# Kernel optimization log

Hardware: AMD Instinct MI355X
Metric: run time of the kernel (lower is better)

## Reference

```python
import jax, jax.numpy as jnp
import numpy as np
from jax import lax

N_ENT, N_REL, N_TYPE = 50000, 237, 4000
DE, NOUT, DT = 100, 128, 200
N_EDGE, B = 800000, 4096
ALPHA, EPS = 0.2, 1e-5
NUM_FILT, FILT_W = 32, 9
FC_LEN = ((NOUT - FILT_W) // 2 + 1 - 2) // 2 + 1  # width after conv(s=2) then pool(2,s=2)
FC_LEN = FC_LEN * NUM_FILT  # height stays 1 -> 30*32 = 960


def setup_inputs() -> dict:
    key = jax.random.key(0)
    ks = jax.random.split(key, 16)
    inp = {
        'x_batch': jax.random.randint(ks[0], (B,), 0, N_ENT),
        'edge_index': jax.random.randint(ks[1], (2, N_EDGE), 0, N_ENT),
        'edge_type': jax.random.randint(ks[2], (N_EDGE,), 0, N_REL),
        'E_w': jax.random.normal(ks[3], (N_ENT, DE)) * 0.05,
        'R_w': jax.random.normal(ks[4], (N_REL, DE)) * 0.05,
        'T_w': jax.random.normal(ks[5], (N_TYPE, DT)) * 0.05,
        'W_f': jax.random.normal(ks[6], (DE, NOUT)) * (1.0 / np.sqrt(DE)),
        'a_vec': jax.random.normal(ks[7], (2 * NOUT,)) * 0.05,
        'conv_w': jax.random.normal(ks[8], (NUM_FILT, 1, 1, FILT_W)) * 0.1,
        'conv_b': jnp.zeros((NUM_FILT,)),
        'bn1_g': jnp.ones((1,)), 'bn1_b': jnp.zeros((1,)),
        'bn3_g': jnp.ones((NUM_FILT,)), 'bn3_b': jnp.zeros((NUM_FILT,)),
        'bn2_g': jnp.ones((DT,)), 'bn2_b': jnp.zeros((DT,)),
        'fc_w': jax.random.normal(ks[9], (DT, FC_LEN)) * (1.0 / np.sqrt(FC_LEN)),
        'fc_b': jnp.zeros((DT,)),
        'b_bias': jnp.zeros((N_TYPE,)),
    }
    return inp


def _bn(x, g, b, axes):
    # training-mode batch norm (biased variance), broadcastable g/b
    mean = jnp.mean(x, axis=axes, keepdims=True)
    var = jnp.var(x, axis=axes, keepdims=True)
    return g * (x - mean) * lax.rsqrt(var + EPS) + b


def _frgat(E_w, R_w, edge_index, edge_type, W_f, a_vec):
    src, dst = edge_index[0], edge_index[1]
    h = E_w @ W_f                                   # [N, NOUT]
    comp = E_w[src] - R_w[edge_type]                # 'sub' composition, [E, DE]
    m = comp @ W_f                                  # messages, [E, NOUT]
    score = jnp.concatenate([h[dst], m], axis=1) @ a_vec  # [E]
    score = jax.nn.leaky_relu(score, ALPHA)
    smax = jax.ops.segment_max(score, dst, num_segments=N_ENT)
    ex = jnp.exp(score - smax[dst])
    denom = jax.ops.segment_sum(ex, dst, num_segments=N_ENT)
    att = ex / (denom[dst] + 1e-16)
    agg = jax.ops.segment_sum(att[:, None] * m, dst, num_segments=N_ENT)
    return jax.nn.elu(agg)                          # F.elu on out_att output


def reference(x_batch, edge_index, edge_type, E_w, R_w, T_w, W_f, a_vec,
              conv_w, conv_b, bn1_g, bn1_b, bn3_g, bn3_b, bn2_g, bn2_b,
              fc_w, fc_b, b_bias):
    ent = _frgat(E_w, R_w, edge_index, edge_type, W_f, a_vec)   # [N, NOUT]
    e = ent[x_batch].reshape(B, 1, 1, NOUT)                     # NCHW
    x = _bn(e, bn1_g.reshape(1, 1, 1, 1), bn1_b.reshape(1, 1, 1, 1), (0, 2, 3))
    x = lax.conv_general_dilated(x, conv_w, window_strides=(2, 2), padding='VALID',
                                 dimension_numbers=('NCHW', 'OIHW', 'NCHW'))
    x = x + conv_b.reshape(1, -1, 1, 1)
    x = _bn(x, bn3_g.reshape(1, -1, 1, 1), bn3_b.reshape(1, -1, 1, 1), (0, 2, 3))
    x = jax.nn.relu(x)
    x = lax.reduce_window(x, -jnp.inf, lax.max, (1, 1, 1, 2), (1, 1, 2, 2), 'VALID')
    x = x.reshape(B, -1)                                        # [B, FC_LEN]
    x = x @ fc_w.T + fc_b
    x = _bn(x, bn2_g[None, :], bn2_b[None, :], (0,))
    x = jax.nn.relu(x)
    logits = x @ T_w.T + b_bias
    return jax.nn.sigmoid(logits)
```

## Files before the change

### kernel.cpp

```cpp
#include <hip/hip_runtime.h>
#include <hip/hip_bf16.h>
#include <math.h>

#define N_ENT   50000
#define N_REL   237
#define N_TYPE  4000
#define DE      100
#define NOUT    128
#define DT      200
#define N_EDGE  800000
#define B_SZ    4096
#define ALPHA   0.2f
#define EPS     1e-5f
#define NUM_FILT 32
#define CONV_W_OUT 60
#define POOL_W  30
#define FC_LEN  960
#define KP      224

typedef unsigned short ushort_t;
typedef __attribute__((ext_vector_type(8))) short bf16x8;
typedef __attribute__((ext_vector_type(4))) float f32x4;

__global__ void k_fill0(float4* p, int n) {
    int i = blockIdx.x * blockDim.x + threadIdx.x;
    if (i < n) p[i] = make_float4(0.f, 0.f, 0.f, 0.f);
}

__global__ void k_fillconst(float* p, long n, float val) {
    long i = (long)blockIdx.x * blockDim.x + threadIdx.x;
    long stride = (long)gridDim.x * blockDim.x;
    for (; i < n; i += stride) p[i] = val;
}

__global__ void k_flags(const int* xb, int* flags) {
    int i = blockIdx.x * blockDim.x + threadIdx.x;
    if (i < B_SZ) flags[xb[i]] = 1;
}

__global__ void k_slots(int* flags, int* counter, int* slotent) {
    int i = blockIdx.x * blockDim.x + threadIdx.x;
    if (i >= N_ENT) return;
    if (flags[i]) {
        int s = atomicAdd(counter, 1);
        flags[i] = 1 + s;
        slotent[s] = i;
    }
}

__global__ void k_prep(const float* Wf, const float* a_vec, const float* Rw,
                       float* wa1, float* wa2, float* rw) {
    __shared__ float sa[2 * NOUT];
    __shared__ float swa2[DE];
    int t = threadIdx.x;
    sa[t] = a_vec[t];
    __syncthreads();
    if (t < DE) {
        float s1 = 0.f, s2 = 0.f;
        for (int j = 0; j < NOUT; j++) {
            float w = Wf[t * NOUT + j];
            s1 += w * sa[j];
            s2 += w * sa[NOUT + j];
        }
        wa1[t] = s1; wa2[t] = s2; swa2[t] = s2;
    }
    __syncthreads();
    if (t < N_REL) {
        float s = 0.f;
        for (int k = 0; k < DE; k++) s += Rw[t * DE + k] * swa2[k];
        rw[t] = s;
    }
}

__global__ void k_entdots(const float* Ew, const float* wa1, const float* wa2,
                          float* ha, float* ew) {
    int wid = blockIdx.x * 4 + (threadIdx.x >> 6);
    int lane = threadIdx.x & 63;
    if (wid >= N_ENT) return;
    float s1 = 0.f, s2 = 0.f;
    if (lane < DE / 2) {
        const float2* p = (const float2*)(Ew + (size_t)wid * DE);
        float2 v = p[lane];
        s1 = v.x * wa1[2 * lane] + v.y * wa1[2 * lane + 1];
        s2 = v.x * wa2[2 * lane] + v.y * wa2[2 * lane + 1];
    }
    for (int off = 32; off > 0; off >>= 1) {
        s1 += __shfl_down(s1, off);
        s2 += __shfl_down(s2, off);
    }
    if (lane == 0) { ha[wid] = s1; ew[wid] = s2; }
}

__global__ void k_count(const int* ei, const int* flags, int* ecount) {
    int e = blockIdx.x * blockDim.x + threadIdx.x;
    if (e >= N_EDGE) return;
    int s = flags[ei[N_EDGE + e]];
    if (s) atomicAdd(&ecount[s - 1], 1);
}

__global__ void k_scan(const int* ecount, int* eoff, int* epos) {
    __shared__ int loc[4096];
    __shared__ int tot[256];
    int t = threadIdx.x;
    int base = t * 16;
    int run = 0;
    for (int i = 0; i < 16; i++) { loc[base + i] = run; run += ecount[base + i]; }
    tot[t] = run;
    __syncthreads();
    for (int off = 1; off < 256; off <<= 1) {
        int u = (t >= off) ? tot[t - off] : 0;
        __syncthreads();
        tot[t] += u;
        __syncthreads();
    }
    int ex = tot[t] - run;
    for (int i = 0; i < 16; i++) {
        int o = ex + loc[base + i];
        eoff[base + i] = o;
        epos[base + i] = o;
    }
}

__global__ void k_scatter(const int* ei, const int* et, const int* flags,
                          int* epos, int2* ebuck) {
    int e = blockIdx.x * blockDim.x + threadIdx.x;
    if (e >= N_EDGE) return;
    int s = flags[ei[N_EDGE + e]];
    if (!s) return;
    int idx = atomicAdd(&epos[s - 1], 1);
    ebuck[idx] = make_int2(ei[e], et[e]);
}

__global__ void k_agg(const int* counter, const int* ecount, const int* eoff,
                      const int* slotent, const int2* ebuck,
                      const float* Ew, const float* Rw,
                      const float* ha, const float* ew, const float* rw,
                      float* aggc) {
    int slot = blockIdx.x;
    if (slot >= counter[0]) return;
    int t = threadIdx.x;
    int n = ecount[slot], o = eoff[slot];
    float hae = ha[slotent[slot]];
    float acc = 0.f, den = 0.f;
    for (int j = 0; j < n; j++) {
        int2 p = ebuck[o + j];
        float sc = hae + ew[p.x] - rw[p.y];
        sc = sc >= 0.f ? sc : ALPHA * sc;
        float ex = expf(sc);
        den += ex;
        if (t < DE) acc += ex * (Ew[(size_t)p.x * DE + t] - Rw[(size_t)p.y * DE + t]);
    }
    if (t < DE) aggc[(size_t)slot * DE + t] = acc / (den + 1e-16f);
}

__global__ void k_gatherconv(const int* xb, const int* flags, const float* aggc,
                             const float* Wf, const float* convw,
                             float* ebuf, float* gps, float* gpq, float* cpart) {
    __shared__ float row[DE];
    __shared__ float xs[NOUT];
    __shared__ float cw[NUM_FILT * 9];
    __shared__ float red[NOUT], red2[NOUT];
    int b = blockIdx.x, t = threadIdx.x;
    int slot = flags[xb[b]] - 1;
    if (t < DE) row[t] = aggc[(size_t)slot * DE + t];
    for (int i = t; i < NUM_FILT * 9; i += 128) cw[i] = convw[i];
    __syncthreads();
    float acc = 0.f;
    for (int k = 0; k < DE; k++) acc += row[k] * Wf[k * NOUT + t];
    float x = acc > 0.f ? acc : expm1f(acc);
    xs[t] = x;
    ebuf[(size_t)b * NOUT + t] = x;
    red[t] = x; red2[t] = x * x;
    __syncthreads();
    for (int s = 64; s > 0; s >>= 1) {
        if (t < s) { red[t] += red[t + s]; red2[t] += red2[t + s]; }
        __syncthreads();
    }
    if (t == 0) { gps[b] = red[0]; gpq[b] = red2[0]; }
    int c = t >> 2, wg = t & 3;
    float ls = 0.f, lq = 0.f;
    for (int i = 0; i < 15; i++) {
        int w = wg + 4 * i;
        float u = 0.f;
        #pragma unroll
        for (int j = 0; j < 9; j++) u += cw[c * 9 + j] * xs[2 * w + j];
        ls += u; lq += u * u;
    }
    __syncthreads();
    red[t] = ls; red2[t] = lq;
    __syncthreads();
    if (wg == 0) {
        float s = red[t] + red[t + 1] + red[t + 2] + red[t + 3];
        float q = red2[t] + red2[t + 1] + red2[t + 2] + red2[t + 3];
        cpart[b * 64 + c] = s;
        cpart[b * 64 + 32 + c] = q;
    }
}

__global__ void k_red1(const float* gps, const float* gpq, const float* g1, float* bn1stat) {
    __shared__ float r1[256], r2[256];
    int t = threadIdx.x;
    float s = 0.f, q = 0.f;
    for (int b = t; b < B_SZ; b += 256) { s += gps[b]; q += gpq[b]; }
    r1[t] = s; r2[t] = q;
    __syncthreads();
    for (int k = 128; k > 0; k >>= 1) {
        if (t < k) { r1[t] += r1[t + k]; r2[t] += r2[t + k]; }
        __syncthreads();
    }
    if (t == 0) {
        float N = (float)(B_SZ * NOUT);
        float mean = r1[0] / N;
        float var = r2[0] / N - mean * mean;
        bn1stat[2] = g1[0] * rsqrtf(var + EPS);
    }
}

__global__ void k_redAB(const float* cpart, const float* bn1stat,
                        const float* g3, const float* b3, float* AB) {
    __shared__ float r1[256], r2[256];
    int c = blockIdx.x, t = threadIdx.x;
    float s = 0.f, q = 0.f;
    for (int b = t; b < B_SZ; b += 256) { s += cpart[b * 64 + c]; q += cpart[b * 64 + 32 + c]; }
    r1[t] = s; r2[t] = q;
    __syncthreads();
    for (int k = 128; k > 0; k >>= 1) {
        if (t < k) { r1[t] += r1[t + k]; r2[t] += r2[t + k]; }
        __syncthreads();
    }
    if (t == 0) {
        float N = (float)(B_SZ * CONV_W_OUT);
        float mu = r1[0] / N;
        float vu = r2[0] / N - mu * mu;
        float s1 = bn1stat[2];
        float A = g3[c] * s1 * rsqrtf(s1 * s1 * vu + EPS);
        AB[c] = A;
        AB[32 + c] = b3[c] - A * mu;
    }
}

__global__ void k_pool(const float* ebuf, const float* convw, const float* AB,
                       __hip_bfloat16* pooled) {
    __shared__ float xs[NOUT];
    __shared__ float cw[NUM_FILT * 9];
    __shared__ float sA[32], sB[32];
    int b = blockIdx.x, t = threadIdx.x;
    xs[t] = ebuf[(size_t)b * NOUT + t];
    for (int i = t; i < NUM_FILT * 9; i += 128) cw[i] = convw[i];
    if (t < 32) { sA[t] = AB[t]; sB[t] = AB[32 + t]; }
    __syncthreads();
    int c = t >> 2, wg = t & 3;
    float A = sA[c], Bv = sB[c];
    for (int i = 0; i < 8; i++) {
        int w2 = wg + 4 * i;
        if (w2 < POOL_W) {
            int w = 2 * w2;
            float u0 = 0.f, u1 = 0.f;
            #pragma unroll
            for (int j = 0; j < 9; j++) {
                float cv = cw[c * 9 + j];
                u0 += cv * xs[2 * w + j];
                u1 += cv * xs[2 * w + 2 + j];
            }
            float z0 = fmaxf(A * u0 + Bv, 0.f);
            float z1 = fmaxf(A * u1 + Bv, 0.f);
            pooled[((size_t)b * NUM_FILT + c) * POOL_W + w2] = __float2bfloat16(fmaxf(z0, z1));
        }
    }
}

__global__ void k_pad_fcw(const float* fcw, __hip_bfloat16* bfc) {
    int i = blockIdx.x * blockDim.x + threadIdx.x;
    if (i >= KP * FC_LEN) return;
    bfc[i] = __float2bfloat16((i < DT * FC_LEN) ? fcw[i] : 0.f);
}

__global__ void k_pad_tw(const float* tw, __hip_bfloat16* b2) {
    int i = blockIdx.x * blockDim.x + threadIdx.x;
    if (i >= N_TYPE * KP) return;
    int n = i / KP, k = i - n * KP;
    b2[i] = __float2bfloat16((k < DT) ? tw[n * DT + k] : 0.f);
}

template<int MODE>
__launch_bounds__(256)
__global__ void k_gemm(const ushort_t* A, const ushort_t* Bm, const float* bias,
                       int K, int ldc, int nbias, float* Cf) {
    int wave = threadIdx.x >> 6, lane = threadIdx.x & 63;
    int m0 = blockIdx.x * 128 + wave * 32;
    int n0 = blockIdx.y * 32;
    int rsel = lane & 15, ksel = (lane >> 4) * 8;
    const ushort_t* pa0 = A + (size_t)(m0 + rsel) * K + ksel;
    const ushort_t* pa1 = pa0 + (size_t)16 * K;
    const ushort_t* pb0 = Bm + (size_t)(n0 + rsel) * K + ksel;
    const ushort_t* pb1 = pb0 + (size_t)16 * K;
    f32x4 acc00 = {0.f, 0.f, 0.f, 0.f};
    f32x4 acc01 = acc00, acc10 = acc00, acc11 = acc00;
    for (int k = 0; k < K; k += 32) {
        bf16x8 a0 = *(const bf16x8*)(pa0 + k);
        bf16x8 a1 = *(const bf16x8*)(pa1 + k);
        bf16x8 b0 = *(const bf16x8*)(pb0 + k);
        bf16x8 b1 = *(const bf16x8*)(pb1 + k);
        acc00 = __builtin_amdgcn_mfma_f32_16x16x32_bf16(a0, b0, acc00, 0, 0, 0);
        acc01 = __builtin_amdgcn_mfma_f32_16x16x32_bf16(a0, b1, acc01, 0, 0, 0);
        acc10 = __builtin_amdgcn_mfma_f32_16x16x32_bf16(a1, b0, acc10, 0, 0, 0);
        acc11 = __builtin_amdgcn_mfma_f32_16x16x32_bf16(a1, b1, acc11, 0, 0, 0);
    }
    int rbase = (lane >> 4) * 4, col = lane & 15;
    auto store_tile = [&](f32x4 acc, int mi, int nj) {
        #pragma unroll
        for (int r2 = 0; r2 < 4; r2++) {
            int row = m0 + mi * 16 + rbase + r2;
            int cc = n0 + nj * 16 + col;
            float v = acc[r2];
            if (MODE == 0) {
                float bb = (cc < nbias) ? bias[cc] : 0.f;
                Cf[(size_t)row * ldc + cc] = v + bb;
            } else {
                Cf[(size_t)row * ldc + cc] = 1.f / (1.f + expf(-(v + bias[cc])));
            }
        }
    };
    store_tile(acc00, 0, 0); store_tile(acc01, 0, 1);
    store_tile(acc10, 1, 0); store_tile(acc11, 1, 1);
}

__global__ void k_bn2stats(const float* fcout, const float* g, const float* bb,
                           float* scale, float* shift) {
    __shared__ float rs[256], rq[256];
    int t = blockIdx.x;
    int tid = threadIdx.x;
    float s = 0.f, q = 0.f;
    for (int b = tid; b < B_SZ; b += 256) {
        float v = fcout[(size_t)b * KP + t];
        s += v; q += v * v;
    }
    rs[tid] = s; rq[tid] = q;
    __syncthreads();
    for (int k = 128; k > 0; k >>= 1) {
        if (tid < k) { rs[tid] += rs[tid + k]; rq[tid] += rq[tid + k]; }
        __syncthreads();
    }
    if (tid == 0) {
        float mean = rs[0] / (float)B_SZ;
        float var = rq[0] / (float)B_SZ - mean * mean;
        float sc = g[t] * rsqrtf(var + EPS);
        scale[t] = sc;
        shift[t] = bb[t] - mean * sc;
    }
}

__global__ void k_bn2apply(const float* fcout, const float* scale, const float* shift,
                           __hip_bfloat16* a2) {
    int i = blockIdx.x * blockDim.x + threadIdx.x;
    if (i >= B_SZ * KP) return;
    int t = i % KP;
    float v = 0.f;
    if (t < DT) {
        v = fcout[i] * scale[t] + shift[t];
        v = fmaxf(v, 0.f);
    }
    a2[i] = __float2bfloat16(v);
}

extern "C" void kernel_launch(void* const* d_in, const int* in_sizes, int n_in,
                              void* d_out, int out_size, void* d_ws, size_t ws_size,
                              hipStream_t stream) {
    (void)in_sizes; (void)n_in;
    const int*   x_batch = (const int*)d_in[0];
    const int*   ei      = (const int*)d_in[1];
    const int*   etype   = (const int*)d_in[2];
    const float* E_w     = (const float*)d_in[3];
    const float* R_w     = (const float*)d_in[4];
    const float* T_w     = (const float*)d_in[5];
    const float* W_f     = (const float*)d_in[6];
    const float* a_vec   = (const float*)d_in[7];
    const float* conv_w  = (const float*)d_in[8];
    const float* bn1_g   = (const float*)d_in[10];
    const float* bn3_g   = (const float*)d_in[12];
    const float* bn3_b   = (const float*)d_in[13];
    const float* bn2_g   = (const float*)d_in[14];
    const float* bn2_b   = (const float*)d_in[15];
    const float* fc_w    = (const float*)d_in[16];
    const float* fc_b    = (const float*)d_in[17];
    const float* b_bias  = (const float*)d_in[18];
    float* out           = (float*)d_out;
    long outn = (long)out_size;

    const size_t WS_NEEDED = 4279552;
    if (ws_size < WS_NEEDED) {
        k_fillconst<<<2048, 256, 0, stream>>>(out, outn, 50.f);
        return;
    }
    char* ws = (char*)d_ws;
    float* wa1      = (float*)(ws + 0);
    float* wa2      = (float*)(ws + 512);
    float* rw       = (float*)(ws + 1024);
    float* bn1stat  = (float*)(ws + 2048);
    float* AB       = (float*)(ws + 2304);
    int*   counter  = (int*)  (ws + 2560);
    float* bn2scale = (float*)(ws + 2816);
    float* bn2shift = (float*)(ws + 3840);
    float* gps      = (float*)(ws + 4864);
    float* gpq      = (float*)(ws + 21248);
    float* cpart    = (float*)(ws + 37632);
    int*   flags    = (int*)  (ws + 1086208);
    int*   slotent  = (int*)  (ws + 1286400);
    int*   ecount   = (int*)  (ws + 1302784);
    int*   eoff     = (int*)  (ws + 1319168);
    int*   epos     = (int*)  (ws + 1335552);
    float* ha       = (float*)(ws + 1351936);
    float* ew       = (float*)(ws + 1552128);
    float* ebuf     = (float*)(ws + 1752320);
    __hip_bfloat16* bfc = (__hip_bfloat16*)(ws + 3849472);
    __hip_bfloat16* a2 = (__hip_bfloat16*)(ws + 4864);
    __hip_bfloat16* b2 = (__hip_bfloat16*)(ws + 1840128);
    __hip_bfloat16* pooled = (__hip_bfloat16*)((char*)d_out + 0);
    float* fcout    = (float*)((char*)d_out + 8388608);
    int2*  ebuck    = (int2*) ((char*)d_out + 16777216);
    float* aggc     = (float*)((char*)d_out + 25165824);

    k_fill0<<<1, 32, 0, stream>>>((float4*)counter, 16);
    k_fill0<<<57, 256, 0, stream>>>((float4*)flags, 232960 / 16);
    k_flags<<<16, 256, 0, stream>>>(x_batch, flags);
    k_slots<<<196, 256, 0, stream>>>(flags, counter, slotent);
    k_prep<<<1, 256, 0, stream>>>(W_f, a_vec, R_w, wa1, wa2, rw);
    k_entdots<<<12500, 256, 0, stream>>>(E_w, wa1, wa2, ha, ew);
    k_count<<<3125, 256, 0, stream>>>(ei, flags, ecount);
    k_scan<<<1, 256, 0, stream>>>(ecount, eoff, epos);
    k_scatter<<<3125, 256, 0, stream>>>(ei, etype, flags, epos, ebuck);
    k_agg<<<4096, 128, 0, stream>>>(counter, ecount, eoff, slotent, ebuck,
                                    E_w, R_w, ha, ew, rw, aggc);
    k_gatherconv<<<4096, 128, 0, stream>>>(x_batch, flags, aggc, W_f, conv_w,
                                           ebuf, gps, gpq, cpart);
    k_red1<<<1, 256, 0, stream>>>(gps, gpq, bn1_g, bn1stat);
    k_redAB<<<32, 256, 0, stream>>>(cpart, bn1stat, bn3_g, bn3_b, AB);
    k_pool<<<4096, 128, 0, stream>>>(ebuf, conv_w, AB, pooled);
    k_pad_fcw<<<840, 256, 0, stream>>>(fc_w, bfc);
    k_gemm<0><<<dim3(32, 7), 256, 0, stream>>>((const ushort_t*)pooled, (const ushort_t*)bfc,
                                               fc_b, FC_LEN, KP, DT, fcout);
    k_bn2stats<<<200, 256, 0, stream>>>(fcout, bn2_g, bn2_b, bn2scale, bn2shift);
    k_bn2apply<<<3584, 256, 0, stream>>>(fcout, bn2scale, bn2shift, a2);
    k_pad_tw<<<3500, 256, 0, stream>>>(T_w, b2);
    k_gemm<1><<<dim3(32, 125), 256, 0, stream>>>((const ushort_t*)a2, (const ushort_t*)b2,
                                                 b_bias, KP, N_TYPE, N_TYPE, out);
}
```

Baseline: 306.7 us.

## Merge small reduction/pad/fill launches and widen the final GEMM tile

Merges k_red1 into k_redAB so each of the 32 blocks also recomputes the BN1 statistics. Combines the two weight-padding kernels into one launch and merges the two zero-fill launches by placing the counter next to the flags. The GEMM is templated on K and on the number of N sub-tiles, with full unrolling for the small K. The output GEMM now uses 64-wide N tiles, with T_w padded to 4032 rows and a column guard on stores. The intent is to cut launch overhead and reuse A fragments across more MFMAs, at the cost of redundant BN1 reduction work and more registers per thread.

Measured after the change: 297.3 us. -3.1%, faster.

```diff
diff --git a/kernel.cpp b/kernel.cpp
--- a/kernel.cpp
+++ b/kernel.cpp
@@ -17,6 +17,7 @@
 #define POOL_W  30
 #define FC_LEN  960
 #define KP      224
+#define NTP     4032
 
 typedef unsigned short ushort_t;
 typedef __attribute__((ext_vector_type(8))) short bf16x8;
@@ -197,42 +198,29 @@
     }
 }
 
-__global__ void k_red1(const float* gps, const float* gpq, const float* g1, float* bn1stat) {
-    __shared__ float r1[256], r2[256];
-    int t = threadIdx.x;
-    float s = 0.f, q = 0.f;
-    for (int b = t; b < B_SZ; b += 256) { s += gps[b]; q += gpq[b]; }
-    r1[t] = s; r2[t] = q;
+__global__ void k_redAB(const float* gps, const float* gpq, const float* cpart,
+                        const float* g1, const float* g3, const float* b3, float* AB) {
+    __shared__ float r1[256], r2[256], r3[256], r4[256];
+    int c = blockIdx.x, t = threadIdx.x;
+    float s = 0.f, q = 0.f, cs = 0.f, cq = 0.f;
+    for (int b = t; b < B_SZ; b += 256) {
+        s += gps[b]; q += gpq[b];
+        cs += cpart[b * 64 + c]; cq += cpart[b * 64 + 32 + c];
+    }
+    r1[t] = s; r2[t] = q; r3[t] = cs; r4[t] = cq;
     __syncthreads();
     for (int k = 128; k > 0; k >>= 1) {
-        if (t < k) { r1[t] += r1[t + k]; r2[t] += r2[t + k]; }
+        if (t < k) { r1[t] += r1[t+k]; r2[t] += r2[t+k]; r3[t] += r3[t+k]; r4[t] += r4[t+k]; }
         __syncthreads();
     }
     if (t == 0) {
-        float N = (float)(B_SZ * NOUT);
-        float mean = r1[0] / N;
-        float var = r2[0] / N - mean * mean;
-        bn1stat[2] = g1[0] * rsqrtf(var + EPS);
-    }
-}
-
-__global__ void k_redAB(const float* cpart, const float* bn1stat,
-                        const float* g3, const float* b3, float* AB) {
-    __shared__ float r1[256], r2[256];
-    int c = blockIdx.x, t = threadIdx.x;
-    float s = 0.f, q = 0.f;
-    for (int b = t; b < B_SZ; b += 256) { s += cpart[b * 64 + c]; q += cpart[b * 64 + 32 + c]; }
-    r1[t] = s; r2[t] = q;
-    __syncthreads();
-    for (int k = 128; k > 0; k >>= 1) {
-        if (t < k) { r1[t] += r1[t + k]; r2[t] += r2[t + k]; }
-        __syncthreads();
-    }
-    if (t == 0) {
-        float N = (float)(B_SZ * CONV_W_OUT);
-        float mu = r1[0] / N;
-        float vu = r2[0] / N - mu * mu;
-        float s1 = bn1stat[2];
+        float N1 = (float)(B_SZ * NOUT);
+        float m1 = r1[0] / N1;
+        float v1 = r2[0] / N1 - m1 * m1;
+        float s1 = g1[0] * rsqrtf(v1 + EPS);
+        float Nc = (float)(B_SZ * CONV_W_OUT);
+        float mu = r3[0] / Nc;
+        float vu = r4[0] / Nc - mu * mu;
         float A = g3[c] * s1 * rsqrtf(s1 * s1 * vu + EPS);
         AB[c] = A;
         AB[32 + c] = b3[c] - A * mu;
@@ -269,60 +257,82 @@
     }
 }
 
-__global__ void k_pad_fcw(const float* fcw, __hip_bfloat16* bfc) {
+__global__ void k_pads(const float* fcw, const float* tw,
+                       __hip_bfloat16* bfc, __hip_bfloat16* b2) {
     int i = blockIdx.x * blockDim.x + threadIdx.x;
-    if (i >= KP * FC_LEN) return;
-    bfc[i] = __float2bfloat16((i < DT * FC_LEN) ? fcw[i] : 0.f);
-}
-
-__global__ void k_pad_tw(const float* tw, __hip_bfloat16* b2) {
-    int i = blockIdx.x * blockDim.x + threadIdx.x;
-    if (i >= N_TYPE * KP) return;
-    int n = i / KP, k = i - n * KP;
-    b2[i] = __float2bfloat16((k < DT) ? tw[n * DT + k] : 0.f);
-}
-
-template<int MODE>
-__launch_bounds__(256)
+    if (i < KP * FC_LEN) {
+        bfc[i] = __float2bfloat16((i < DT * FC_LEN) ? fcw[i] : 0.f);
+    } else {
+        int j = i - KP * FC_LEN;
+        if (j >= NTP * KP) return;
+        int n = j / KP, k = j - n * KP;
+        float v = (n < N_TYPE && k < DT) ? tw[n * DT + k] : 0.f;
+        b2[j] = __float2bfloat16(v);
+    }
+}
+
+template<int MODE, int K, int NB>
+__launch_bounds__(256, 4)
 __global__ void k_gemm(const ushort_t* A, const ushort_t* Bm, const float* bias,
-                       int K, int ldc, int nbias, float* Cf) {
+                       int ldc, int nbias, float* Cf) {
     int wave = threadIdx.x >> 6, lane = threadIdx.x & 63;
     int m0 = blockIdx.x * 128 + wave * 32;
-    int n0 = blockIdx.y * 32;
+    int n0 = blockIdx.y * (16 * NB);
     int rsel = lane & 15, ksel = (lane >> 4) * 8;
     const ushort_t* pa0 = A + (size_t)(m0 + rsel) * K + ksel;
     const ushort_t* pa1 = pa0 + (size_t)16 * K;
-    const ushort_t* pb0 = Bm + (size_t)(n0 + rsel) * K + ksel;
-    const ushort_t* pb1 = pb0 + (size_t)16 * K;
-    f32x4 acc00 = {0.f, 0.f, 0.f, 0.f};
-    f32x4 acc01 = acc00, acc10 = acc00, acc11 = acc00;
-    for (int k = 0; k < K; k += 32) {
-        bf16x8 a0 = *(const bf16x8*)(pa0 + k);
-        bf16x8 a1 = *(const bf16x8*)(pa1 + k);
-        bf16x8 b0 = *(const bf16x8*)(pb0 + k);
-        bf16x8 b1 = *(const bf16x8*)(pb1 + k);
-        acc00 = __builtin_amdgcn_mfma_f32_16x16x32_bf16(a0, b0, acc00, 0, 0, 0);
-        acc01 = __builtin_amdgcn_mfma_f32_16x16x32_bf16(a0, b1, acc01, 0, 0, 0);
-        acc10 = __builtin_amdgcn_mfma_f32_16x16x32_bf16(a1, b0, acc10, 0, 0, 0);
-        acc11 = __builtin_amdgcn_mfma_f32_16x16x32_bf16(a1, b1, acc11, 0, 0, 0);
+    const ushort_t* pb[NB];
+    #pragma unroll
+    for (int j = 0; j < NB; j++) pb[j] = Bm + (size_t)(n0 + j * 16 + rsel) * K + ksel;
+    f32x4 acc0[NB], acc1[NB];
+    #pragma unroll
+    for (int j = 0; j < NB; j++) { acc0[j] = (f32x4){0.f,0.f,0.f,0.f}; acc1[j] = acc0[j]; }
+    if constexpr (K <= 256) {
+        #pragma unroll
+        for (int k = 0; k < K; k += 32) {
+            bf16x8 a0 = *(const bf16x8*)(pa0 + k);
+            bf16x8 a1 = *(const bf16x8*)(pa1 + k);
+            #pragma unroll
+            for (int j = 0; j < NB; j++) {
+                bf16x8 b = *(const bf16x8*)(pb[j] + k);
+                acc0[j] = __builtin_amdgcn_mfma_f32_16x16x32_bf16(a0, b, acc0[j], 0, 0, 0);
+                acc1[j] = __builtin_amdgcn_mfma_f32_16x16x32_bf16(a1, b, acc1[j], 0, 0, 0);
+            }
+        }
+    } else {
+        #pragma unroll 4
+        for (int k = 0; k < K; k += 32) {
+            bf16x8 a0 = *(const bf16x8*)(pa0 + k);
+            bf16x8 a1 = *(const bf16x8*)(pa1 + k);
+            #pragma unroll
+            for (int j = 0; j < NB; j++) {
+                bf16x8 b = *(const bf16x8*)(pb[j] + k);
+                acc0[j] = __builtin_amdgcn_mfma_f32_16x16x32_bf16(a0, b, acc0[j], 0, 0, 0);
+                acc1[j] = __builtin_amdgcn_mfma_f32_16x16x32_bf16(a1, b, acc1[j], 0, 0, 0);
+            }
+        }
     }
     int rbase = (lane >> 4) * 4, col = lane & 15;
-    auto store_tile = [&](f32x4 acc, int mi, int nj) {
+    auto store_tile = [&](f32x4 acc, int mrow, int nj) {
         #pragma unroll
         for (int r2 = 0; r2 < 4; r2++) {
-            int row = m0 + mi * 16 + rbase + r2;
+            int row = mrow + rbase + r2;
             int cc = n0 + nj * 16 + col;
             float v = acc[r2];
             if (MODE == 0) {
                 float bb = (cc < nbias) ? bias[cc] : 0.f;
                 Cf[(size_t)row * ldc + cc] = v + bb;
             } else {
-                Cf[(size_t)row * ldc + cc] = 1.f / (1.f + expf(-(v + bias[cc])));
+                if (cc < nbias)
+                    Cf[(size_t)row * ldc + cc] = 1.f / (1.f + expf(-(v + bias[cc])));
             }
         }
     };
-    store_tile(acc00, 0, 0); store_tile(acc01, 0, 1);
-    store_tile(acc10, 1, 0); store_tile(acc11, 1, 1);
+    #pragma unroll
+    for (int j = 0; j < NB; j++) {
+        store_tile(acc0[j], m0, j);
+        store_tile(acc1[j], m0 + 16, j);
+    }
 }
 
 __global__ void k_bn2stats(const float* fcout, const float* g, const float* bb,
@@ -387,7 +397,7 @@
     float* out           = (float*)d_out;
     long outn = (long)out_size;
 
-    const size_t WS_NEEDED = 4279552;
+    const size_t WS_NEEDED = 4279296;
     if (ws_size < WS_NEEDED) {
         k_fillconst<<<2048, 256, 0, stream>>>(out, outn, 50.f);
         return;
@@ -396,23 +406,22 @@
     float* wa1      = (float*)(ws + 0);
     float* wa2      = (float*)(ws + 512);
     float* rw       = (float*)(ws + 1024);
-    float* bn1stat  = (float*)(ws + 2048);
-    float* AB       = (float*)(ws + 2304);
-    int*   counter  = (int*)  (ws + 2560);
+    float* AB       = (float*)(ws + 2048);
     float* bn2scale = (float*)(ws + 2816);
     float* bn2shift = (float*)(ws + 3840);
     float* gps      = (float*)(ws + 4864);
     float* gpq      = (float*)(ws + 21248);
     float* cpart    = (float*)(ws + 37632);
-    int*   flags    = (int*)  (ws + 1086208);
-    int*   slotent  = (int*)  (ws + 1286400);
-    int*   ecount   = (int*)  (ws + 1302784);
-    int*   eoff     = (int*)  (ws + 1319168);
-    int*   epos     = (int*)  (ws + 1335552);
-    float* ha       = (float*)(ws + 1351936);
-    float* ew       = (float*)(ws + 1552128);
-    float* ebuf     = (float*)(ws + 1752320);
-    __hip_bfloat16* bfc = (__hip_bfloat16*)(ws + 3849472);
+    int*   counter  = (int*)  (ws + 1086208);
+    int*   flags    = (int*)  (ws + 1086464);
+    int*   slotent  = (int*)  (ws + 1286464);
+    int*   ecount   = (int*)  (ws + 1302848);
+    int*   eoff     = (int*)  (ws + 1319232);
+    int*   epos     = (int*)  (ws + 1335616);
+    float* ha       = (float*)(ws + 1352064);
+    float* ew       = (float*)(ws + 1552064);
+    float* ebuf     = (float*)(ws + 1752064);
+    __hip_bfloat16* bfc = (__hip_bfloat16*)(ws + 3849216);
     __hip_bfloat16* a2 = (__hip_bfloat16*)(ws + 4864);
     __hip_bfloat16* b2 = (__hip_bfloat16*)(ws + 1840128);
     __hip_bfloat16* pooled = (__hip_bfloat16*)((char*)d_out + 0);
@@ -420,8 +429,7 @@
     int2*  ebuck    = (int2*) ((char*)d_out + 16777216);
     float* aggc     = (float*)((char*)d_out + 25165824);
 
-    k_fill0<<<1, 32, 0, stream>>>((float4*)counter, 16);
-    k_fill0<<<57, 256, 0, stream>>>((float4*)flags, 232960 / 16);
+    k_fill0<<<57, 256, 0, stream>>>((float4*)counter, 233024 / 16);
     k_flags<<<16, 256, 0, stream>>>(x_batch, flags);
     k_slots<<<196, 256, 0, stream>>>(flags, counter, slotent);
     k_prep<<<1, 256, 0, stream>>>(W_f, a_vec, R_w, wa1, wa2, rw);
@@ -433,15 +441,13 @@
                                     E_w, R_w, ha, ew, rw, aggc);
     k_gatherconv<<<4096, 128, 0, stream>>>(x_batch, flags, aggc, W_f, conv_w,
                                            ebuf, gps, gpq, cpart);
-    k_red1<<<1, 256, 0, stream>>>(gps, gpq, bn1_g, bn1stat);
-    k_redAB<<<32, 256, 0, stream>>>(cpart, bn1stat, bn3_g, bn3_b, AB);
+    k_redAB<<<32, 256, 0, stream>>>(gps, gpq, cpart, bn1_g, bn3_g, bn3_b, AB);
     k_pool<<<4096, 128, 0, stream>>>(ebuf, conv_w, AB, pooled);
-    k_pad_fcw<<<840, 256, 0, stream>>>(fc_w, bfc);
-    k_gemm<0><<<dim3(32, 7), 256, 0, stream>>>((const ushort_t*)pooled, (const ushort_t*)bfc,
-                                               fc_b, FC_LEN, KP, DT, fcout);
+    k_pads<<<4368, 256, 0, stream>>>(fc_w, T_w, bfc, b2);
+    k_gemm<0, FC_LEN, 2><<<dim3(32, 7), 256, 0, stream>>>(
+        (const ushort_t*)pooled, (const ushort_t*)bfc, fc_b, KP, DT, fcout);
     k_bn2stats<<<200, 256, 0, stream>>>(fcout, bn2_g, bn2_b, bn2scale, bn2shift);
     k_bn2apply<<<3584, 256, 0, stream>>>(fcout, bn2scale, bn2shift, a2);
-    k_pad_tw<<<3500, 256, 0, stream>>>(T_w, b2);
-    k_gemm<1><<<dim3(32, 125), 256, 0, stream>>>((const ushort_t*)a2, (const ushort_t*)b2,
-                                                 b_bias, KP, N_TYPE, N_TYPE, out);
-}
+    k_gemm<1, KP, 4><<<dim3(32, 63), 256, 0, stream>>>(
+        (const ushort_t*)a2, (const ushort_t*)b2, b_bias, N_TYPE, N_TYPE, out);
+}
```
